# Kernel tuning notes

Hardware: AMD Instinct MI355X
Metric: run time of the kernel (lower is better)

## Reference

```python
import jax, jax.numpy as jnp
import numpy as np

DIM = 128
N_ROUNDS = 120


def _mlp(x, W1, b1, W2, b2, W3, b3):
    h = jax.nn.relu(x @ W1.T + b1)
    h = jax.nn.relu(h @ W2.T + b2)
    return h @ W3.T + b3


def _lstm(x, h, c, Wih, Whh, bih, bhh):
    # torch nn.LSTM gate order: i, f, g, o
    g = x @ Wih.T + h @ Whh.T + (bih + bhh)
    i, f, gg, o = jnp.split(g, 4, axis=-1)
    c2 = jax.nn.sigmoid(f) * c + jax.nn.sigmoid(i) * jnp.tanh(gg)
    h2 = jax.nn.sigmoid(o) * jnp.tanh(c2)
    return h2, c2


def setup_inputs() -> dict:
    key = jax.random.key(0)
    keys = iter(jax.random.split(key, 64))
    def w(*shape):
        return jax.random.normal(next(keys), shape, dtype=jnp.float32) * 0.05
    n_nodes, n_vars = 8000, 1000
    N = n_nodes + n_vars
    # sparse 0/1 adjacency, stored dense as in the original (adj_matrix.values)
    adj = (jax.random.uniform(next(keys), (n_nodes, N)) < 0.003).astype(jnp.float32)
    values = jax.random.randint(next(keys), (N,), 0, 2)
    inp = dict(adj=adj, values=values, n_nodes=n_nodes)
    inp.update(true_W=w(DIM, 1), true_b=w(DIM), false_W=w(DIM, 1), false_b=w(DIM))
    for p in ("cm", "pm"):
        inp.update({p + "_W1": w(DIM, DIM), p + "_b1": w(DIM),
                    p + "_W2": w(DIM, DIM), p + "_b2": w(DIM),
                    p + "_W3": w(DIM, DIM), p + "_b3": w(DIM)})
    inp.update(vv_W1=w(DIM, DIM), vv_b1=w(DIM), vv_W2=w(DIM, DIM), vv_b2=w(DIM),
               vv_W3=w(1, DIM), vv_b3=w(1))
    for p in ("vu", "nu"):
        inp.update({p + "_Wih": w(4 * DIM, DIM), p + "_Whh": w(4 * DIM, DIM),
                    p + "_bih": w(4 * DIM), p + "_bhh": w(4 * DIM)})
    return inp


def reference(adj, values, n_nodes, true_W, true_b, false_W, false_b,
              cm_W1, cm_b1, cm_W2, cm_b2, cm_W3, cm_b3,
              pm_W1, pm_b1, pm_W2, pm_b2, pm_W3, pm_b3,
              vv_W1, vv_b1, vv_W2, vv_b2, vv_W3, vv_b3,
              vu_Wih, vu_Whh, vu_bih, vu_bhh,
              nu_Wih, nu_Whh, nu_bih, nu_bhh):
    init_ts = jnp.ones((1,), jnp.float32)
    true_vec = true_W @ init_ts + true_b     # (128,)
    false_vec = false_W @ init_ts + false_b  # (128,)
    h0 = jnp.where((values == 1)[:, None], true_vec, false_vec)  # (N,128)
    c0 = jnp.zeros_like(h0)

    def step(carry, _):
        h, c = carry
        var_pre = _mlp(h, cm_W1, cm_b1, cm_W2, cm_b2, cm_W3, cm_b3)   # (N,128)
        c2p = adj @ var_pre                                           # (n_nodes,128)
        hn, cn = _lstm(c2p, h[:n_nodes], c[:n_nodes], vu_Wih, vu_Whh, vu_bih, vu_bhh)
        h = jnp.concatenate([hn, h[n_nodes:]], axis=0)
        c = jnp.concatenate([cn, c[n_nodes:]], axis=0)
        node_pre = _mlp(h[:n_nodes], pm_W1, pm_b1, pm_W2, pm_b2, pm_W3, pm_b3)
        p2c = adj.T @ node_pre                                        # (N,128)
        h, c = _lstm(p2c, h, c, nu_Wih, nu_Whh, nu_bih, nu_bhh)
        return (h, c), None

    (h, c), _ = jax.lax.scan(step, (h0, c0), None, length=N_ROUNDS)
    vote = _mlp(h[n_nodes:], vv_W1, vv_b1, vv_W2, vv_b2, vv_W3, vv_b3)  # (n_vars,1)
    return vote.squeeze(-1)
```

## Files before the change

### kernel.cpp

```cpp
#include <hip/hip_runtime.h>
#include <cstddef>
#include <cstdint>

#define DIM 128
#define NROUNDS 120
#define NNZ_CAP (1 << 20)

typedef _Float16 half8 __attribute__((ext_vector_type(8)));
typedef float f32x4 __attribute__((ext_vector_type(4)));
typedef unsigned long long u64;

__device__ __forceinline__ float sigf(float x) { return 1.f / (1.f + __expf(-x)); }
__device__ __forceinline__ float tanh_fast(float x) { return 2.f / (1.f + __expf(-2.f * x)) - 1.f; }

__global__ void count_nz_kernel(const float* __restrict__ adj, int* __restrict__ row_cnt,
                                int* __restrict__ col_cnt, int ncols) {
  int i = blockIdx.x;
  int j = blockIdx.y * blockDim.x + threadIdx.x;
  bool nz = (j < ncols) && (adj[(size_t)i * ncols + j] != 0.f);
  unsigned long long m = __ballot(nz);
  if ((threadIdx.x & 63) == 0) {
    int c = __popcll(m);
    if (c) atomicAdd(&row_cnt[i], c);
  }
  if (nz) atomicAdd(&col_cnt[j], 1);
}

__global__ void scan_kernel(const int* __restrict__ cnt, int* __restrict__ ptr, int n) {
  __shared__ int sdata[256];
  int t = threadIdx.x;
  int per = (n + 255) / 256;
  int beg = t * per;
  int end = beg + per; if (end > n) end = n;
  int local = 0;
  for (int i = beg; i < end; ++i) local += cnt[i];
  sdata[t] = local;
  __syncthreads();
  for (int off = 1; off < 256; off <<= 1) {
    int v = (t >= off) ? sdata[t - off] : 0;
    __syncthreads();
    sdata[t] += v;
    __syncthreads();
  }
  int run = sdata[t] - local;
  for (int i = beg; i < end; ++i) { ptr[i] = run; run += cnt[i]; }
  if (t == 255) ptr[n] = sdata[255];
}

__global__ __launch_bounds__(64) void fill_csr_kernel(const float* __restrict__ adj,
                                                      const int* __restrict__ row_ptr,
                                                      int* __restrict__ col_idx, int ncols) {
  int row = blockIdx.x;
  int lane = threadIdx.x;
  int base = row_ptr[row];
  int cursor = 0;
  const float* arow = adj + (size_t)row * ncols;
  for (int j0 = 0; j0 < ncols; j0 += 64) {
    int j = j0 + lane;
    bool nz = (j < ncols) && (arow[j] != 0.f);
    u64 m = __ballot(nz);
    int pre = __popcll(m & ((1ull << lane) - 1));
    if (nz) col_idx[base + cursor + pre] = j;
    cursor += __popcll(m);
  }
}

__global__ __launch_bounds__(64) void fill_csc_kernel(const float* __restrict__ adj,
                                                      const int* __restrict__ col_ptr,
                                                      int* __restrict__ row_idx,
                                                      int nrows, int ncols) {
  int c = blockIdx.x * 64 + threadIdx.x;
  if (c >= ncols) return;
  int cur = col_ptr[c];
  for (int i = 0; i < nrows; ++i) {
    if (adj[(size_t)i * ncols + c] != 0.f) row_idx[cur++] = i;
  }
}

__global__ void pack_w_kernel(const float* __restrict__ src, int out_dim,
                              _Float16* __restrict__ dh) {
  int idx = blockIdx.x * 256 + threadIdx.x;
  if (idx >= out_dim * DIM) return;
  int n = idx >> 7, k = idx & 127;
  _Float16 hi = (_Float16)src[idx];
  int nt = n >> 4, ks = k >> 5;
  int L = ((k >> 3) & 3) * 16 + (n & 15);
  int j = k & 7;
  dh[((nt * 4 + ks) * 64 + L) * 8 + j] = hi;
}

__global__ void pack_bias_kernel(const float* __restrict__ a, const float* __restrict__ b,
                                 float* __restrict__ o, int n) {
  int i = blockIdx.x * 256 + threadIdx.x;
  if (i < n) o[i] = a[i] + b[i];
}

__global__ void init_hc_kernel(const int* __restrict__ values, const float* __restrict__ tW,
                               const float* __restrict__ tb, const float* __restrict__ fW,
                               const float* __restrict__ fb, float* __restrict__ h,
                               float* __restrict__ c, int N) {
  int idx = blockIdx.x * blockDim.x + threadIdx.x;
  if (idx >= N * DIM) return;
  int row = idx >> 7, col = idx & (DIM - 1);
  float tv = tW[col] + tb[col];
  float fv = fW[col] + fb[col];
  h[idx] = (values[row] == 1) ? tv : fv;
  c[idx] = 0.f;
}

__device__ __forceinline__ int sw_idx(int m, int k) {
  return (m << 7) + (((((k >> 3) ^ (m & 15))) << 3) | (k & 7));
}

__device__ __forceinline__ float touch(const _Float16* __restrict__ w, int n, int tid) {
  float t = 0.f;
  for (int i = tid * 64; i < n; i += 512 * 64) t += (float)w[i];
  return t;
}

template <int NSUB>
__device__ __forceinline__ void stage_rows_t(const float* __restrict__ src, int rend, int rb,
                                             _Float16* Sh, _Float16* Sl, int tid) {
  int seg = tid & 15;
  for (int r = tid >> 4; r < NSUB * 16; r += 32) {
    int row = rb + r;
    float4 v0, v1;
    if (row < rend) {
      const float4* s = (const float4*)(src + (size_t)row * DIM + seg * 8);
      v0 = s[0]; v1 = s[1];
    } else {
      v0.x = v0.y = v0.z = v0.w = 0.f; v1 = v0;
    }
    int a = sw_idx(r, seg * 8);
    float vv[8] = {v0.x, v0.y, v0.z, v0.w, v1.x, v1.y, v1.z, v1.w};
#pragma unroll
    for (int e = 0; e < 8; ++e) {
      _Float16 hi = (_Float16)vv[e];
      Sh[a + e] = hi;
      Sl[a + e] = (_Float16)(vv[e] - (float)hi);
    }
  }
}

template <int NSUB>
__device__ __forceinline__ void gather_rows_t(const int* __restrict__ ptr,
                                              const int* __restrict__ nzidx,
                                              const _Float16* __restrict__ va, int rend, int rb,
                                              _Float16* Xh, _Float16* Xl, int tid) {
  int seg = tid & 15;
  for (int r = tid >> 4; r < NSUB * 16; r += 32) {
    int row = rb + r;
    float a[8];
#pragma unroll
    for (int e = 0; e < 8; ++e) a[e] = 0.f;
    if (row < rend) {
      int s = ptr[row], e_ = ptr[row + 1];
      int p = s;
      for (; p + 8 <= e_; p += 8) {
        half8 v0 = *(const half8*)(va + (size_t)nzidx[p] * DIM + seg * 8);
        half8 v1 = *(const half8*)(va + (size_t)nzidx[p + 1] * DIM + seg * 8);
        half8 v2 = *(const half8*)(va + (size_t)nzidx[p + 2] * DIM + seg * 8);
        half8 v3 = *(const half8*)(va + (size_t)nzidx[p + 3] * DIM + seg * 8);
        half8 v4 = *(const half8*)(va + (size_t)nzidx[p + 4] * DIM + seg * 8);
        half8 v5 = *(const half8*)(va + (size_t)nzidx[p + 5] * DIM + seg * 8);
        half8 v6 = *(const half8*)(va + (size_t)nzidx[p + 6] * DIM + seg * 8);
        half8 v7 = *(const half8*)(va + (size_t)nzidx[p + 7] * DIM + seg * 8);
#pragma unroll
        for (int e = 0; e < 8; ++e)
          a[e] += (((float)v0[e] + (float)v1[e]) + ((float)v2[e] + (float)v3[e])) +
                  (((float)v4[e] + (float)v5[e]) + ((float)v6[e] + (float)v7[e]));
      }
      for (; p + 2 <= e_; p += 2) {
        half8 v0 = *(const half8*)(va + (size_t)nzidx[p] * DIM + seg * 8);
        half8 v1 = *(const half8*)(va + (size_t)nzidx[p + 1] * DIM + seg * 8);
#pragma unroll
        for (int e = 0; e < 8; ++e) a[e] += (float)v0[e] + (float)v1[e];
      }
      if (p < e_) {
        half8 v = *(const half8*)(va + (size_t)nzidx[p] * DIM + seg * 8);
#pragma unroll
        for (int e = 0; e < 8; ++e) a[e] += (float)v[e];
      }
    }
    int aoff = sw_idx(r, seg * 8);
#pragma unroll
    for (int e = 0; e < 8; ++e) {
      _Float16 hi = (_Float16)a[e];
      Xh[aoff + e] = hi;
      Xl[aoff + e] = (_Float16)(a[e] - (float)hi);
    }
  }
}

__device__ __forceinline__ void mfma2(f32x4& acc, half8 ah, half8 al, half8 bh) {
  acc = __builtin_amdgcn_mfma_f32_16x16x32_f16(ah, bh, acc, 0, 0, 0);
  acc = __builtin_amdgcn_mfma_f32_16x16x32_f16(al, bh, acc, 0, 0, 0);
}

template <int NSUB>
__device__ __forceinline__ void mlp_layer_t(const _Float16* Ah_, const _Float16* Al_,
                                            const _Float16* __restrict__ Wh,
                                            const float* __restrict__ B,
                                            _Float16* Dh, _Float16* Dl, int tid) {
  int lane = tid & 63, w = tid >> 6;
  int m16 = lane & 15, quad = lane >> 4;
  float bv = B[w * 16 + m16];
  f32x4 acc[NSUB];
#pragma unroll
  for (int s = 0; s < NSUB; ++s) acc[s] = (f32x4){bv, bv, bv, bv};
#pragma unroll
  for (int ks = 0; ks < 4; ++ks) {
    int boff = ((w * 4 + ks) * 64 + lane) * 8;
    half8 bh = *(const half8*)(Wh + boff);
#pragma unroll
    for (int s = 0; s < NSUB; ++s) {
      int a_off = sw_idx(s * 16 + m16, ks * 32 + quad * 8);
      mfma2(acc[s], *(const half8*)(Ah_ + a_off), *(const half8*)(Al_ + a_off), bh);
    }
  }
#pragma unroll
  for (int s = 0; s < NSUB; ++s)
#pragma unroll
    for (int reg = 0; reg < 4; ++reg) {
      int rl = s * 16 + quad * 4 + reg;
      int col = w * 16 + m16;
      float x = fmaxf(acc[s][reg], 0.f);
      _Float16 hi = (_Float16)x;
      int a = sw_idx(rl, col);
      Dh[a] = hi;
      Dl[a] = (_Float16)(x - (float)hi);
    }
  __syncthreads();
}

template <int NSUB>
__device__ __forceinline__ void mlp_from_lds_t(
    _Float16* S0, _Float16* S1, _Float16* S2, _Float16* S3, int rend, int rb,
    const _Float16* __restrict__ W1h, const float* __restrict__ b1,
    const _Float16* __restrict__ W2h, const float* __restrict__ b2,
    const _Float16* __restrict__ W3h, const float* __restrict__ b3,
    _Float16* __restrict__ out) {
  int tid = threadIdx.x;
  mlp_layer_t<NSUB>(S0, S1, W1h, b1, S2, S3, tid);
  mlp_layer_t<NSUB>(S2, S3, W2h, b2, S0, S1, tid);
  int lane = tid & 63, w = tid >> 6;
  int m16 = lane & 15, quad = lane >> 4;
  float bv = b3[w * 16 + m16];
  f32x4 acc[NSUB];
#pragma unroll
  for (int s = 0; s < NSUB; ++s) acc[s] = (f32x4){bv, bv, bv, bv};
#pragma unroll
  for (int ks = 0; ks < 4; ++ks) {
    int boff = ((w * 4 + ks) * 64 + lane) * 8;
    half8 bh = *(const half8*)(W3h + boff);
#pragma unroll
    for (int s = 0; s < NSUB; ++s) {
      int a_off = sw_idx(s * 16 + m16, ks * 32 + quad * 8);
      mfma2(acc[s], *(const half8*)(S0 + a_off), *(const half8*)(S1 + a_off), bh);
    }
  }
#pragma unroll
  for (int s = 0; s < NSUB; ++s)
#pragma unroll
    for (int reg = 0; reg < 4; ++reg) {
      int row = rb + s * 16 + quad * 4 + reg;
      int col = w * 16 + m16;
      if (row < rend) out[(size_t)row * DIM + col] = (_Float16)acc[s][reg];
    }
}

template <int NSUB>
__global__ __launch_bounds__(512, 4) void mlp3_mfma(
    const float* __restrict__ X, int M, int rpb,
    const _Float16* __restrict__ W1h, const float* __restrict__ b1,
    const _Float16* __restrict__ W2h, const float* __restrict__ b2,
    const _Float16* __restrict__ W3h, const float* __restrict__ b3,
    _Float16* __restrict__ out) {
  __shared__ _Float16 S0[NSUB * 2048], S1[NSUB * 2048], S2[NSUB * 2048], S3[NSUB * 2048];
  int tid = threadIdx.x;
  int rb = blockIdx.x * rpb;
  int rend = rb + rpb; if (rend > M) rend = M;
  float tpf = touch(W1h, DIM * DIM, tid) + touch(W2h, DIM * DIM, tid) + touch(W3h, DIM * DIM, tid);
  stage_rows_t<NSUB>(X, rend, rb, S0, S1, tid);
  asm volatile("" :: "v"(tpf));
  __syncthreads();
  mlp_from_lds_t<NSUB>(S0, S1, S2, S3, rend, rb, W1h, b1, W2h, b2, W3h, b3, out);
}

template <int NSUB, bool DO_MLP>
__global__ __launch_bounds__(512, 4) void lstm_fused(
    const int* __restrict__ ptr, const int* __restrict__ nzidx, const _Float16* __restrict__ va_in,
    float* __restrict__ hbuf, float* __restrict__ cbuf, int M, int rpb,
    const _Float16* __restrict__ Wxh, const _Float16* __restrict__ Whh_,
    const float* __restrict__ bcomb,
    const _Float16* __restrict__ W1h, const float* __restrict__ b1,
    const _Float16* __restrict__ W2h, const float* __restrict__ b2,
    const _Float16* __restrict__ W3h, const float* __restrict__ b3,
    _Float16* __restrict__ va_out) {
  __shared__ _Float16 Xh[NSUB * 2048], Xl[NSUB * 2048], Hh[NSUB * 2048], Hl[NSUB * 2048];
  int tid = threadIdx.x;
  int rb = blockIdx.x * rpb;
  int rend = rb + rpb; if (rend > M) rend = M;

  float tpf = touch(Wxh, 4 * DIM * DIM, tid) + touch(Whh_, 4 * DIM * DIM, tid) +
              touch(W1h, DIM * DIM, tid) + touch(W2h, DIM * DIM, tid) + touch(W3h, DIM * DIM, tid);

  stage_rows_t<NSUB>(hbuf, rend, rb, Hh, Hl, tid);
  gather_rows_t<NSUB>(ptr, nzidx, va_in, rend, rb, Xh, Xl, tid);

  int lane = tid & 63, w = tid >> 6;
  int m16 = lane & 15, quad = lane >> 4;

  float cold[NSUB][4];
#pragma unroll
  for (int s = 0; s < NSUB; ++s)
#pragma unroll
    for (int reg = 0; reg < 4; ++reg) {
      int row = rb + s * 16 + quad * 4 + reg;
      cold[s][reg] = (row < rend) ? cbuf[(size_t)row * DIM + w * 16 + m16] : 0.f;
    }
  asm volatile("" :: "v"(tpf));
  __syncthreads();

  f32x4 acc[NSUB][4];
#pragma unroll
  for (int g = 0; g < 4; ++g) {
    float bv = bcomb[g * 128 + w * 16 + m16];
#pragma unroll
    for (int s = 0; s < NSUB; ++s) acc[s][g] = (f32x4){bv, bv, bv, bv};
  }
#pragma unroll
  for (int ks = 0; ks < 4; ++ks) {
#pragma unroll
    for (int g = 0; g < 4; ++g) {
      int ct = g * 8 + w;
      int boff = ((ct * 4 + ks) * 64 + lane) * 8;
      half8 bh = *(const half8*)(Whh_ + boff);
#pragma unroll
      for (int s = 0; s < NSUB; ++s) {
        int a_off = sw_idx(s * 16 + m16, ks * 32 + quad * 8);
        mfma2(acc[s][g], *(const half8*)(Hh + a_off), *(const half8*)(Hl + a_off), bh);
      }
    }
  }
#pragma unroll
  for (int ks = 0; ks < 4; ++ks) {
#pragma unroll
    for (int g = 0; g < 4; ++g) {
      int ct = g * 8 + w;
      int boff = ((ct * 4 + ks) * 64 + lane) * 8;
      half8 bh = *(const half8*)(Wxh + boff);
#pragma unroll
      for (int s = 0; s < NSUB; ++s) {
        int a_off = sw_idx(s * 16 + m16, ks * 32 + quad * 8);
        mfma2(acc[s][g], *(const half8*)(Xh + a_off), *(const half8*)(Xl + a_off), bh);
      }
    }
  }

  if (DO_MLP) __syncthreads();

#pragma unroll
  for (int s = 0; s < NSUB; ++s)
#pragma unroll
    for (int reg = 0; reg < 4; ++reg) {
      int rl = s * 16 + quad * 4 + reg;
      int row = rb + rl;
      int col = w * 16 + m16;
      float hn = 0.f;
      if (row < rend) {
        float iv = sigf(acc[s][0][reg]);
        float fv = sigf(acc[s][1][reg]);
        float gv = tanh_fast(acc[s][2][reg]);
        float ov = sigf(acc[s][3][reg]);
        size_t o = (size_t)row * DIM + col;
        float cn = fv * cold[s][reg] + iv * gv;
        cbuf[o] = cn;
        hn = ov * tanh_fast(cn);
        hbuf[o] = hn;
      }
      if (DO_MLP) {
        int a = sw_idx(rl, col);
        _Float16 hi = (_Float16)hn;
        Xh[a] = hi;
        Xl[a] = (_Float16)(hn - (float)hi);
      }
    }
  if (DO_MLP) {
    __syncthreads();
    mlp_from_lds_t<NSUB>(Xh, Xl, Hh, Hl, rend, rb, W1h, b1, W2h, b2, W3h, b3, va_out);
  }
}

__device__ __forceinline__ void tile_gemm(const float* S, const float* __restrict__ W,
                                          int colB, int rowB, float acc[4][4]) {
#pragma unroll 4
  for (int kc = 0; kc < DIM; kc += 4) {
    float4 xv[4], wv[4];
#pragma unroll
    for (int r = 0; r < 4; ++r) xv[r] = *(const float4*)(S + (rowB + r) * DIM + kc);
#pragma unroll
    for (int c = 0; c < 4; ++c) wv[c] = *(const float4*)(W + (size_t)(colB + c) * DIM + kc);
#pragma unroll
    for (int r = 0; r < 4; ++r)
#pragma unroll
      for (int c = 0; c < 4; ++c)
        acc[r][c] += xv[r].x * wv[c].x + xv[r].y * wv[c].y + xv[r].z * wv[c].z + xv[r].w * wv[c].w;
  }
}

__device__ __forceinline__ void layer_lds(const float* Sin, float* Sout,
                                          const float* __restrict__ W, const float* __restrict__ B,
                                          bool relu, int colB, int rowB) {
  float acc[4][4];
#pragma unroll
  for (int r = 0; r < 4; ++r)
#pragma unroll
    for (int cc = 0; cc < 4; ++cc) acc[r][cc] = B[colB + cc];
  tile_gemm(Sin, W, colB, rowB, acc);
#pragma unroll
  for (int r = 0; r < 4; ++r) {
    float4 v;
    v.x = acc[r][0]; v.y = acc[r][1]; v.z = acc[r][2]; v.w = acc[r][3];
    if (relu) { v.x = fmaxf(v.x, 0.f); v.y = fmaxf(v.y, 0.f); v.z = fmaxf(v.z, 0.f); v.w = fmaxf(v.w, 0.f); }
    *(float4*)&Sout[(rowB + r) * DIM + colB] = v;
  }
  __syncthreads();
}

__global__ __launch_bounds__(256) void vote_kernel(
    const float* __restrict__ X, int M,
    const float* __restrict__ W1, const float* __restrict__ b1,
    const float* __restrict__ W2, const float* __restrict__ b2,
    const float* __restrict__ W3, const float* __restrict__ b3,
    float* __restrict__ out) {
  __shared__ float Xs[32 * DIM];
  __shared__ float Ys[32 * DIM];
  int tid = threadIdx.x;
  int rb = blockIdx.x * 32;
  int mrows = M - rb; if (mrows > 32) mrows = 32;
  {
    const float4* src = (const float4*)(X + (size_t)rb * DIM);
    float4* dst = (float4*)Xs;
    int nf4 = mrows * (DIM / 4);
    for (int t = tid; t < 32 * (DIM / 4); t += 256) {
      float4 v;
      if (t < nf4) v = src[t];
      else { v.x = v.y = v.z = v.w = 0.f; }
      dst[t] = v;
    }
  }
  __syncthreads();
  int tx = tid & 31, ty = tid >> 5;
  int colB = tx * 4, rowB = ty * 4;
  layer_lds(Xs, Ys, W1, b1, true, colB, rowB);
  layer_lds(Ys, Xs, W2, b2, true, colB, rowB);
  if (tid < 32) {
    int gr = rb + tid;
    if (gr < M) {
      float s = b3[0];
      for (int k = 0; k < DIM; ++k) s += Xs[tid * DIM + k] * W3[k];
      out[gr] = s;
    }
  }
}

#define SZ128 (DIM * DIM)
#define SZ512 (4 * DIM * DIM)
#define O_CM1 0
#define O_CM2 (SZ128)
#define O_CM3 (2 * SZ128)
#define O_PM1 (3 * SZ128)
#define O_PM2 (4 * SZ128)
#define O_PM3 (5 * SZ128)
#define O_VUX ((size_t)6 * SZ128)
#define O_VUH ((size_t)6 * SZ128 + SZ512)
#define O_NUX ((size_t)6 * SZ128 + 2 * SZ512)
#define O_NUH ((size_t)6 * SZ128 + 3 * SZ512)

extern "C" void kernel_launch(void* const* d_in, const int* in_sizes, int n_in,
                              void* d_out, int out_size, void* d_ws, size_t ws_size,
                              hipStream_t stream) {
  const float* adj    = (const float*)d_in[0];
  const int*   values = (const int*)d_in[1];
  const int N       = in_sizes[1];
  const int n_nodes = in_sizes[0] / N;
  const int n_vars  = N - n_nodes;

  const float* true_W  = (const float*)d_in[3];
  const float* true_b  = (const float*)d_in[4];
  const float* false_W = (const float*)d_in[5];
  const float* false_b = (const float*)d_in[6];
  const float* cm_W1 = (const float*)d_in[7];
  const float* cm_b1 = (const float*)d_in[8];
  const float* cm_W2 = (const float*)d_in[9];
  const float* cm_b2 = (const float*)d_in[10];
  const float* cm_W3 = (const float*)d_in[11];
  const float* cm_b3 = (const float*)d_in[12];
  const float* pm_W1 = (const float*)d_in[13];
  const float* pm_b1 = (const float*)d_in[14];
  const float* pm_W2 = (const float*)d_in[15];
  const float* pm_b2 = (const float*)d_in[16];
  const float* pm_W3 = (const float*)d_in[17];
  const float* pm_b3 = (const float*)d_in[18];
  const float* vv_W1 = (const float*)d_in[19];
  const float* vv_b1 = (const float*)d_in[20];
  const float* vv_W2 = (const float*)d_in[21];
  const float* vv_b2 = (const float*)d_in[22];
  const float* vv_W3 = (const float*)d_in[23];
  const float* vv_b3 = (const float*)d_in[24];
  const float* vu_Wih = (const float*)d_in[25];
  const float* vu_Whh = (const float*)d_in[26];
  const float* vu_bih = (const float*)d_in[27];
  const float* vu_bhh = (const float*)d_in[28];
  const float* nu_Wih = (const float*)d_in[29];
  const float* nu_Whh = (const float*)d_in[30];
  const float* nu_bih = (const float*)d_in[31];
  const float* nu_bhh = (const float*)d_in[32];

  uintptr_t p = (uintptr_t)d_ws;
  auto take = [&](size_t bytes) -> void* {
    uintptr_t cur = (p + 255) & ~(uintptr_t)255;
    p = cur + bytes;
    return (void*)cur;
  };
  float* h   = (float*)take((size_t)N * DIM * sizeof(float));
  float* cb  = (float*)take((size_t)N * DIM * sizeof(float));
  _Float16* va1 = (_Float16*)take((size_t)N * DIM * sizeof(_Float16));
  _Float16* va2 = (_Float16*)take((size_t)N * DIM * sizeof(_Float16));
  int* row_ptr = (int*)take((size_t)(n_nodes + 1) * sizeof(int));
  int* col_ptr = (int*)take((size_t)(N + 1) * sizeof(int));
  int* cnts    = (int*)take((size_t)(n_nodes + N) * sizeof(int));
  int* row_cnt = cnts;
  int* col_cnt = cnts + n_nodes;
  int* col_idx = (int*)take((size_t)NNZ_CAP * sizeof(int));
  int* row_idx = (int*)take((size_t)NNZ_CAP * sizeof(int));

  size_t tot_pack = (size_t)6 * SZ128 + (size_t)4 * SZ512;
  _Float16* packh = (_Float16*)take(tot_pack * sizeof(_Float16));
  float* vu_b = (float*)take(512 * sizeof(float));
  float* nu_b = (float*)take(512 * sizeof(float));

  hipMemsetAsync(cnts, 0, (size_t)(n_nodes + N) * sizeof(int), stream);
  dim3 cgrid(n_nodes, (N + 255) / 256);
  count_nz_kernel<<<cgrid, 256, 0, stream>>>(adj, row_cnt, col_cnt, N);
  scan_kernel<<<1, 256, 0, stream>>>(row_cnt, row_ptr, n_nodes);
  scan_kernel<<<1, 256, 0, stream>>>(col_cnt, col_ptr, N);
  fill_csr_kernel<<<n_nodes, 64, 0, stream>>>(adj, row_ptr, col_idx, N);
  fill_csc_kernel<<<(N + 63) / 64, 64, 0, stream>>>(adj, col_ptr, row_idx, n_nodes, N);
  init_hc_kernel<<<(N * DIM + 255) / 256, 256, 0, stream>>>(values, true_W, true_b,
                                                            false_W, false_b, h, cb, N);

  auto pack = [&](const float* src, int out_dim, size_t o) {
    pack_w_kernel<<<(out_dim * DIM + 255) / 256, 256, 0, stream>>>(src, out_dim, packh + o);
  };
  pack(cm_W1, DIM, O_CM1); pack(cm_W2, DIM, O_CM2); pack(cm_W3, DIM, O_CM3);
  pack(pm_W1, DIM, O_PM1); pack(pm_W2, DIM, O_PM2); pack(pm_W3, DIM, O_PM3);
  pack(vu_Wih, 4 * DIM, O_VUX); pack(vu_Whh, 4 * DIM, O_VUH);
  pack(nu_Wih, 4 * DIM, O_NUX); pack(nu_Whh, 4 * DIM, O_NUH);
  pack_bias_kernel<<<2, 256, 0, stream>>>(vu_bih, vu_bhh, vu_b, 512);
  pack_bias_kernel<<<2, 256, 0, stream>>>(nu_bih, nu_bhh, nu_b, 512);

  int rpbN = (N + 499) / 500;
  int gridN = (N + rpbN - 1) / rpbN;
  int rpbn = (n_nodes + 499) / 500;
  int gridn = (n_nodes + rpbn - 1) / rpbn;

  mlp3_mfma<2><<<gridN, 512, 0, stream>>>(h, N, rpbN,
      packh + O_CM1, cm_b1, packh + O_CM2, cm_b2, packh + O_CM3, cm_b3, va1);

  for (int r = 0; r < NROUNDS; ++r) {
    lstm_fused<1, true><<<gridn, 512, 0, stream>>>(row_ptr, col_idx, va1, h, cb, n_nodes, rpbn,
        packh + O_VUX, packh + O_VUH, vu_b,
        packh + O_PM1, pm_b1, packh + O_PM2, pm_b2, packh + O_PM3, pm_b3, va2);
    if (r + 1 < NROUNDS) {
      lstm_fused<2, true><<<gridN, 512, 0, stream>>>(col_ptr, row_idx, va2, h, cb, N, rpbN,
          packh + O_NUX, packh + O_NUH, nu_b,
          packh + O_CM1, cm_b1, packh + O_CM2, cm_b2, packh + O_CM3, cm_b3, va1);
    } else {
      lstm_fused<2, false><<<gridN, 512, 0, stream>>>(col_ptr, row_idx, va2, h, cb, N, rpbN,
          packh + O_NUX, packh + O_NUH, nu_b,
          packh + O_CM1, cm_b1, packh + O_CM2, cm_b2, packh + O_CM3, cm_b3, va1);
    }
  }

  vote_kernel<<<(n_vars + 31) / 32, 256, 0, stream>>>(h + (size_t)n_nodes * DIM, n_vars,
      vv_W1, vv_b1, vv_W2, vv_b2, vv_W3, vv_b3, (float*)d_out);
}
```

Measured before the change: 10.05 ms.

## Replace per-round kernel launches with a persistent kernel using grid barriers

```diff
diff --git a/kernel.cpp b/kernel.cpp
--- a/kernel.cpp
+++ b/kernel.cpp
@@ -5,6 +5,7 @@
 #define DIM 128
 #define NROUNDS 120
 #define NNZ_CAP (1 << 20)
+#define NB 250
 
 typedef _Float16 half8 __attribute__((ext_vector_type(8)));
 typedef float f32x4 __attribute__((ext_vector_type(4)));
@@ -16,14 +17,23 @@
 __global__ void count_nz_kernel(const float* __restrict__ adj, int* __restrict__ row_cnt,
                                 int* __restrict__ col_cnt, int ncols) {
   int i = blockIdx.x;
-  int j = blockIdx.y * blockDim.x + threadIdx.x;
-  bool nz = (j < ncols) && (adj[(size_t)i * ncols + j] != 0.f);
-  unsigned long long m = __ballot(nz);
-  if ((threadIdx.x & 63) == 0) {
-    int c = __popcll(m);
-    if (c) atomicAdd(&row_cnt[i], c);
-  }
-  if (nz) atomicAdd(&col_cnt[j], 1);
+  int t4 = blockIdx.y * blockDim.x + threadIdx.x;
+  int j0 = t4 * 4;
+  int c = 0;
+  if (j0 < ncols) {
+    if ((ncols & 3) == 0) {
+      float4 v = *(const float4*)(adj + (size_t)i * ncols + j0);
+      if (v.x != 0.f) { atomicAdd(&col_cnt[j0 + 0], 1); ++c; }
+      if (v.y != 0.f) { atomicAdd(&col_cnt[j0 + 1], 1); ++c; }
+      if (v.z != 0.f) { atomicAdd(&col_cnt[j0 + 2], 1); ++c; }
+      if (v.w != 0.f) { atomicAdd(&col_cnt[j0 + 3], 1); ++c; }
+    } else {
+      for (int e = 0; e < 4 && j0 + e < ncols; ++e)
+        if (adj[(size_t)i * ncols + j0 + e] != 0.f) { atomicAdd(&col_cnt[j0 + e], 1); ++c; }
+    }
+  }
+  for (int off = 32; off; off >>= 1) c += __shfl_down(c, off, 64);
+  if ((threadIdx.x & 63) == 0 && c) atomicAdd(&row_cnt[i], c);
 }
 
 __global__ void scan_kernel(const int* __restrict__ cnt, int* __restrict__ ptr, int n) {
@@ -47,9 +57,16 @@
   if (t == 255) ptr[n] = sdata[255];
 }
 
-__global__ __launch_bounds__(64) void fill_csr_kernel(const float* __restrict__ adj,
-                                                      const int* __restrict__ row_ptr,
-                                                      int* __restrict__ col_idx, int ncols) {
+__global__ void copy_int_kernel(const int* __restrict__ a, int* __restrict__ b, int n) {
+  int i = blockIdx.x * 256 + threadIdx.x;
+  if (i < n) b[i] = a[i];
+}
+
+__global__ __launch_bounds__(64) void fill_csr_csc_kernel(const float* __restrict__ adj,
+                                                          const int* __restrict__ row_ptr,
+                                                          int* __restrict__ col_idx,
+                                                          int* __restrict__ col_cur,
+                                                          int* __restrict__ row_idx, int ncols) {
   int row = blockIdx.x;
   int lane = threadIdx.x;
   int base = row_ptr[row];
@@ -60,20 +77,12 @@
     bool nz = (j < ncols) && (arow[j] != 0.f);
     u64 m = __ballot(nz);
     int pre = __popcll(m & ((1ull << lane) - 1));
-    if (nz) col_idx[base + cursor + pre] = j;
+    if (nz) {
+      col_idx[base + cursor + pre] = j;
+      int t = atomicAdd(&col_cur[j], 1);
+      row_idx[t] = row;
+    }
     cursor += __popcll(m);
-  }
-}
-
-__global__ __launch_bounds__(64) void fill_csc_kernel(const float* __restrict__ adj,
-                                                      const int* __restrict__ col_ptr,
-                                                      int* __restrict__ row_idx,
-                                                      int nrows, int ncols) {
-  int c = blockIdx.x * 64 + threadIdx.x;
-  if (c >= ncols) return;
-  int cur = col_ptr[c];
-  for (int i = 0; i < nrows; ++i) {
-    if (adj[(size_t)i * ncols + c] != 0.f) row_idx[cur++] = i;
   }
 }
 
@@ -95,19 +104,6 @@
   if (i < n) o[i] = a[i] + b[i];
 }
 
-__global__ void init_hc_kernel(const int* __restrict__ values, const float* __restrict__ tW,
-                               const float* __restrict__ tb, const float* __restrict__ fW,
-                               const float* __restrict__ fb, float* __restrict__ h,
-                               float* __restrict__ c, int N) {
-  int idx = blockIdx.x * blockDim.x + threadIdx.x;
-  if (idx >= N * DIM) return;
-  int row = idx >> 7, col = idx & (DIM - 1);
-  float tv = tW[col] + tb[col];
-  float fv = fW[col] + fb[col];
-  h[idx] = (values[row] == 1) ? tv : fv;
-  c[idx] = 0.f;
-}
-
 __device__ __forceinline__ int sw_idx(int m, int k) {
   return (m << 7) + (((((k >> 3) ^ (m & 15))) << 3) | (k & 7));
 }
@@ -118,42 +114,18 @@
   return t;
 }
 
-template <int NSUB>
-__device__ __forceinline__ void stage_rows_t(const float* __restrict__ src, int rend, int rb,
-                                             _Float16* Sh, _Float16* Sl, int tid) {
+template <int NS>
+__device__ __forceinline__ void gather_pers(const int* __restrict__ ptr,
+                                            const int* __restrict__ nzidx,
+                                            const _Float16* __restrict__ va, int rowlim,
+                                            int b, int nb, _Float16* Xh, _Float16* Xl, int tid) {
   int seg = tid & 15;
-  for (int r = tid >> 4; r < NSUB * 16; r += 32) {
-    int row = rb + r;
-    float4 v0, v1;
-    if (row < rend) {
-      const float4* s = (const float4*)(src + (size_t)row * DIM + seg * 8);
-      v0 = s[0]; v1 = s[1];
-    } else {
-      v0.x = v0.y = v0.z = v0.w = 0.f; v1 = v0;
-    }
-    int a = sw_idx(r, seg * 8);
-    float vv[8] = {v0.x, v0.y, v0.z, v0.w, v1.x, v1.y, v1.z, v1.w};
-#pragma unroll
-    for (int e = 0; e < 8; ++e) {
-      _Float16 hi = (_Float16)vv[e];
-      Sh[a + e] = hi;
-      Sl[a + e] = (_Float16)(vv[e] - (float)hi);
-    }
-  }
-}
-
-template <int NSUB>
-__device__ __forceinline__ void gather_rows_t(const int* __restrict__ ptr,
-                                              const int* __restrict__ nzidx,
-                                              const _Float16* __restrict__ va, int rend, int rb,
-                                              _Float16* Xh, _Float16* Xl, int tid) {
-  int seg = tid & 15;
-  for (int r = tid >> 4; r < NSUB * 16; r += 32) {
-    int row = rb + r;
+  for (int r = tid >> 4; r < NS * 16; r += 32) {
+    int row = b + r * nb;
     float a[8];
 #pragma unroll
     for (int e = 0; e < 8; ++e) a[e] = 0.f;
-    if (row < rend) {
+    if (row < rowlim) {
       int s = ptr[row], e_ = ptr[row + 1];
       int p = s;
       for (; p + 8 <= e_; p += 8) {
@@ -197,7 +169,7 @@
   acc = __builtin_amdgcn_mfma_f32_16x16x32_f16(al, bh, acc, 0, 0, 0);
 }
 
-template <int NSUB>
+template <int NS>
 __device__ __forceinline__ void mlp_layer_t(const _Float16* Ah_, const _Float16* Al_,
                                             const _Float16* __restrict__ Wh,
                                             const float* __restrict__ B,
@@ -205,21 +177,21 @@
   int lane = tid & 63, w = tid >> 6;
   int m16 = lane & 15, quad = lane >> 4;
   float bv = B[w * 16 + m16];
-  f32x4 acc[NSUB];
-#pragma unroll
-  for (int s = 0; s < NSUB; ++s) acc[s] = (f32x4){bv, bv, bv, bv};
+  f32x4 acc[NS];
+#pragma unroll
+  for (int s = 0; s < NS; ++s) acc[s] = (f32x4){bv, bv, bv, bv};
 #pragma unroll
   for (int ks = 0; ks < 4; ++ks) {
     int boff = ((w * 4 + ks) * 64 + lane) * 8;
     half8 bh = *(const half8*)(Wh + boff);
 #pragma unroll
-    for (int s = 0; s < NSUB; ++s) {
+    for (int s = 0; s < NS; ++s) {
       int a_off = sw_idx(s * 16 + m16, ks * 32 + quad * 8);
       mfma2(acc[s], *(const half8*)(Ah_ + a_off), *(const half8*)(Al_ + a_off), bh);
     }
   }
 #pragma unroll
-  for (int s = 0; s < NSUB; ++s)
+  for (int s = 0; s < NS; ++s)
 #pragma unroll
     for (int reg = 0; reg < 4; ++reg) {
       int rl = s * 16 + quad * 4 + reg;
@@ -233,162 +205,262 @@
   __syncthreads();
 }
 
-template <int NSUB>
-__device__ __forceinline__ void mlp_from_lds_t(
-    _Float16* S0, _Float16* S1, _Float16* S2, _Float16* S3, int rend, int rb,
-    const _Float16* __restrict__ W1h, const float* __restrict__ b1,
-    const _Float16* __restrict__ W2h, const float* __restrict__ b2,
-    const _Float16* __restrict__ W3h, const float* __restrict__ b3,
-    _Float16* __restrict__ out) {
-  int tid = threadIdx.x;
-  mlp_layer_t<NSUB>(S0, S1, W1h, b1, S2, S3, tid);
-  mlp_layer_t<NSUB>(S2, S3, W2h, b2, S0, S1, tid);
+template <int NS>
+__device__ __forceinline__ void mlp_pers(const _Float16* Ah, const _Float16* Al,
+                                         _Float16* T1h, _Float16* T1l,
+                                         _Float16* T2h, _Float16* T2l,
+                                         const _Float16* __restrict__ W1h, const float* __restrict__ b1,
+                                         const _Float16* __restrict__ W2h, const float* __restrict__ b2,
+                                         const _Float16* __restrict__ W3h, const float* __restrict__ b3,
+                                         _Float16* __restrict__ out, int rowlim, int b, int nb,
+                                         int tid) {
+  mlp_layer_t<NS>(Ah, Al, W1h, b1, T1h, T1l, tid);
+  mlp_layer_t<NS>(T1h, T1l, W2h, b2, T2h, T2l, tid);
   int lane = tid & 63, w = tid >> 6;
   int m16 = lane & 15, quad = lane >> 4;
   float bv = b3[w * 16 + m16];
-  f32x4 acc[NSUB];
-#pragma unroll
-  for (int s = 0; s < NSUB; ++s) acc[s] = (f32x4){bv, bv, bv, bv};
+  f32x4 acc[NS];
+#pragma unroll
+  for (int s = 0; s < NS; ++s) acc[s] = (f32x4){bv, bv, bv, bv};
 #pragma unroll
   for (int ks = 0; ks < 4; ++ks) {
     int boff = ((w * 4 + ks) * 64 + lane) * 8;
     half8 bh = *(const half8*)(W3h + boff);
 #pragma unroll
-    for (int s = 0; s < NSUB; ++s) {
+    for (int s = 0; s < NS; ++s) {
       int a_off = sw_idx(s * 16 + m16, ks * 32 + quad * 8);
-      mfma2(acc[s], *(const half8*)(S0 + a_off), *(const half8*)(S1 + a_off), bh);
-    }
-  }
-#pragma unroll
-  for (int s = 0; s < NSUB; ++s)
+      mfma2(acc[s], *(const half8*)(T2h + a_off), *(const half8*)(T2l + a_off), bh);
+    }
+  }
+#pragma unroll
+  for (int s = 0; s < NS; ++s)
 #pragma unroll
     for (int reg = 0; reg < 4; ++reg) {
-      int row = rb + s * 16 + quad * 4 + reg;
+      int rl = s * 16 + quad * 4 + reg;
+      int row = b + rl * nb;
       int col = w * 16 + m16;
-      if (row < rend) out[(size_t)row * DIM + col] = (_Float16)acc[s][reg];
-    }
-}
-
-template <int NSUB>
-__global__ __launch_bounds__(512, 4) void mlp3_mfma(
-    const float* __restrict__ X, int M, int rpb,
-    const _Float16* __restrict__ W1h, const float* __restrict__ b1,
-    const _Float16* __restrict__ W2h, const float* __restrict__ b2,
-    const _Float16* __restrict__ W3h, const float* __restrict__ b3,
-    _Float16* __restrict__ out) {
-  __shared__ _Float16 S0[NSUB * 2048], S1[NSUB * 2048], S2[NSUB * 2048], S3[NSUB * 2048];
-  int tid = threadIdx.x;
-  int rb = blockIdx.x * rpb;
-  int rend = rb + rpb; if (rend > M) rend = M;
-  float tpf = touch(W1h, DIM * DIM, tid) + touch(W2h, DIM * DIM, tid) + touch(W3h, DIM * DIM, tid);
-  stage_rows_t<NSUB>(X, rend, rb, S0, S1, tid);
-  asm volatile("" :: "v"(tpf));
-  __syncthreads();
-  mlp_from_lds_t<NSUB>(S0, S1, S2, S3, rend, rb, W1h, b1, W2h, b2, W3h, b3, out);
-}
-
-template <int NSUB, bool DO_MLP>
-__global__ __launch_bounds__(512, 4) void lstm_fused(
-    const int* __restrict__ ptr, const int* __restrict__ nzidx, const _Float16* __restrict__ va_in,
-    float* __restrict__ hbuf, float* __restrict__ cbuf, int M, int rpb,
-    const _Float16* __restrict__ Wxh, const _Float16* __restrict__ Whh_,
-    const float* __restrict__ bcomb,
-    const _Float16* __restrict__ W1h, const float* __restrict__ b1,
-    const _Float16* __restrict__ W2h, const float* __restrict__ b2,
-    const _Float16* __restrict__ W3h, const float* __restrict__ b3,
-    _Float16* __restrict__ va_out) {
-  __shared__ _Float16 Xh[NSUB * 2048], Xl[NSUB * 2048], Hh[NSUB * 2048], Hl[NSUB * 2048];
-  int tid = threadIdx.x;
-  int rb = blockIdx.x * rpb;
-  int rend = rb + rpb; if (rend > M) rend = M;
-
-  float tpf = touch(Wxh, 4 * DIM * DIM, tid) + touch(Whh_, 4 * DIM * DIM, tid) +
-              touch(W1h, DIM * DIM, tid) + touch(W2h, DIM * DIM, tid) + touch(W3h, DIM * DIM, tid);
-
-  stage_rows_t<NSUB>(hbuf, rend, rb, Hh, Hl, tid);
-  gather_rows_t<NSUB>(ptr, nzidx, va_in, rend, rb, Xh, Xl, tid);
-
+      if (row < rowlim) out[(size_t)row * DIM + col] = (_Float16)acc[s][reg];
+    }
+}
+
+template <int NS>
+__device__ __forceinline__ void lstm_pers(const _Float16* Hh, const _Float16* Hl,
+                                          const _Float16* Xh, const _Float16* Xl,
+                                          const _Float16* __restrict__ Wxh,
+                                          const _Float16* __restrict__ Whh_,
+                                          const float* __restrict__ bcomb, int tid,
+                                          f32x4 (&acc)[NS][4]) {
   int lane = tid & 63, w = tid >> 6;
   int m16 = lane & 15, quad = lane >> 4;
-
-  float cold[NSUB][4];
-#pragma unroll
-  for (int s = 0; s < NSUB; ++s)
-#pragma unroll
-    for (int reg = 0; reg < 4; ++reg) {
-      int row = rb + s * 16 + quad * 4 + reg;
-      cold[s][reg] = (row < rend) ? cbuf[(size_t)row * DIM + w * 16 + m16] : 0.f;
-    }
-  asm volatile("" :: "v"(tpf));
-  __syncthreads();
-
-  f32x4 acc[NSUB][4];
 #pragma unroll
   for (int g = 0; g < 4; ++g) {
     float bv = bcomb[g * 128 + w * 16 + m16];
 #pragma unroll
-    for (int s = 0; s < NSUB; ++s) acc[s][g] = (f32x4){bv, bv, bv, bv};
+    for (int s = 0; s < NS; ++s) acc[s][g] = (f32x4){bv, bv, bv, bv};
   }
 #pragma unroll
   for (int ks = 0; ks < 4; ++ks) {
+    half8 ah[NS], al[NS];
+#pragma unroll
+    for (int s = 0; s < NS; ++s) {
+      int a_off = sw_idx(s * 16 + m16, ks * 32 + quad * 8);
+      ah[s] = *(const half8*)(Hh + a_off);
+      al[s] = *(const half8*)(Hl + a_off);
+    }
 #pragma unroll
     for (int g = 0; g < 4; ++g) {
-      int ct = g * 8 + w;
-      int boff = ((ct * 4 + ks) * 64 + lane) * 8;
+      int boff = (((g * 8 + w) * 4 + ks) * 64 + lane) * 8;
       half8 bh = *(const half8*)(Whh_ + boff);
 #pragma unroll
-      for (int s = 0; s < NSUB; ++s) {
-        int a_off = sw_idx(s * 16 + m16, ks * 32 + quad * 8);
-        mfma2(acc[s][g], *(const half8*)(Hh + a_off), *(const half8*)(Hl + a_off), bh);
-      }
-    }
-  }
-#pragma unroll
-  for (int ks = 0; ks < 4; ++ks) {
+      for (int s = 0; s < NS; ++s) mfma2(acc[s][g], ah[s], al[s], bh);
+    }
+#pragma unroll
+    for (int s = 0; s < NS; ++s) {
+      int a_off = sw_idx(s * 16 + m16, ks * 32 + quad * 8);
+      ah[s] = *(const half8*)(Xh + a_off);
+      al[s] = *(const half8*)(Xl + a_off);
+    }
 #pragma unroll
     for (int g = 0; g < 4; ++g) {
-      int ct = g * 8 + w;
-      int boff = ((ct * 4 + ks) * 64 + lane) * 8;
+      int boff = (((g * 8 + w) * 4 + ks) * 64 + lane) * 8;
       half8 bh = *(const half8*)(Wxh + boff);
 #pragma unroll
-      for (int s = 0; s < NSUB; ++s) {
-        int a_off = sw_idx(s * 16 + m16, ks * 32 + quad * 8);
-        mfma2(acc[s][g], *(const half8*)(Xh + a_off), *(const half8*)(Xl + a_off), bh);
-      }
-    }
-  }
-
-  if (DO_MLP) __syncthreads();
-
-#pragma unroll
-  for (int s = 0; s < NSUB; ++s)
+      for (int s = 0; s < NS; ++s) mfma2(acc[s][g], ah[s], al[s], bh);
+    }
+  }
+}
+
+__device__ __forceinline__ void gbar(unsigned* __restrict__ cnt, int nblocks, unsigned ep) {
+  __syncthreads();
+  if (threadIdx.x == 0) {
+    __threadfence();
+    __hip_atomic_fetch_add(cnt, 1u, __ATOMIC_RELAXED, __HIP_MEMORY_SCOPE_AGENT);
+    unsigned tgt = ep * (unsigned)nblocks;
+    int guard = 0;
+    while (__hip_atomic_load(cnt, __ATOMIC_RELAXED, __HIP_MEMORY_SCOPE_AGENT) < tgt) {
+      __builtin_amdgcn_s_sleep(8);
+      if (++guard > (1 << 17)) break;
+    }
+    __threadfence();
+  }
+  __syncthreads();
+}
+
+#define SZ128 (DIM * DIM)
+#define SZ512 (4 * DIM * DIM)
+#define O_CM1 0
+#define O_CM2 (SZ128)
+#define O_CM3 (2 * SZ128)
+#define O_PM1 (3 * SZ128)
+#define O_PM2 (4 * SZ128)
+#define O_PM3 (5 * SZ128)
+#define O_VUX ((size_t)6 * SZ128)
+#define O_VUH ((size_t)6 * SZ128 + SZ512)
+#define O_NUX ((size_t)6 * SZ128 + 2 * SZ512)
+#define O_NUH ((size_t)6 * SZ128 + 3 * SZ512)
+
+#define LSLOT (3 * 2048 + 768)
+
+template <int NS1>
+__global__ __launch_bounds__(512, 2) void persist_kernel(
+    const int* __restrict__ row_ptr, const int* __restrict__ col_idx,
+    const int* __restrict__ col_ptr, const int* __restrict__ row_idx,
+    const int* __restrict__ values, const float* __restrict__ tW, const float* __restrict__ tb,
+    const float* __restrict__ fW, const float* __restrict__ fb,
+    const _Float16* __restrict__ packh,
+    const float* __restrict__ vu_b, const float* __restrict__ nu_b,
+    const float* __restrict__ cm_b1, const float* __restrict__ cm_b2,
+    const float* __restrict__ cm_b3, const float* __restrict__ pm_b1,
+    const float* __restrict__ pm_b2, const float* __restrict__ pm_b3,
+    _Float16* __restrict__ va1, _Float16* __restrict__ va2,
+    float* __restrict__ hout, unsigned* __restrict__ bar_cnt,
+    int n_nodes, int N, int nblocks) {
+  __shared__ _Float16 Hh[LSLOT], Hl[LSLOT], Xh[LSLOT], Xl[LSLOT], T2h[LSLOT], T2l[LSLOT];
+  int tid = threadIdx.x, b = blockIdx.x;
+  int lane = tid & 63, w = tid >> 6, m16 = lane & 15, quad = lane >> 4;
+
+  const _Float16* CM1 = packh + O_CM1;
+  const _Float16* CM2 = packh + O_CM2;
+  const _Float16* CM3 = packh + O_CM3;
+  const _Float16* PM1 = packh + O_PM1;
+  const _Float16* PM2 = packh + O_PM2;
+  const _Float16* PM3 = packh + O_PM3;
+  const _Float16* VUX = packh + O_VUX;
+  const _Float16* VUH = packh + O_VUH;
+  const _Float16* NUX = packh + O_NUX;
+  const _Float16* NUH = packh + O_NUH;
+
+  float cold[3][4];
+#pragma unroll
+  for (int s = 0; s < 3; ++s)
 #pragma unroll
     for (int reg = 0; reg < 4; ++reg) {
+      cold[s][reg] = 0.f;
       int rl = s * 16 + quad * 4 + reg;
-      int row = rb + rl;
+      int row = b + rl * nblocks;
       int col = w * 16 + m16;
-      float hn = 0.f;
-      if (row < rend) {
-        float iv = sigf(acc[s][0][reg]);
-        float fv = sigf(acc[s][1][reg]);
-        float gv = tanh_fast(acc[s][2][reg]);
-        float ov = sigf(acc[s][3][reg]);
-        size_t o = (size_t)row * DIM + col;
-        float cn = fv * cold[s][reg] + iv * gv;
-        cbuf[o] = cn;
-        hn = ov * tanh_fast(cn);
-        hbuf[o] = hn;
-      }
-      if (DO_MLP) {
-        int a = sw_idx(rl, col);
-        _Float16 hi = (_Float16)hn;
-        Xh[a] = hi;
-        Xl[a] = (_Float16)(hn - (float)hi);
-      }
-    }
-  if (DO_MLP) {
+      float hv = 0.f;
+      if (row < N) hv = (values[row] == 1) ? (tW[col] + tb[col]) : (fW[col] + fb[col]);
+      int a = sw_idx(rl, col);
+      _Float16 hi = (_Float16)hv;
+      Hh[a] = hi;
+      Hl[a] = (_Float16)(hv - (float)hi);
+    }
+  __syncthreads();
+
+  unsigned ep = 0;
+  {
+    float tpf = touch(CM1, DIM * DIM, tid) + touch(CM2, DIM * DIM, tid) +
+                touch(CM3, DIM * DIM, tid);
+    asm volatile("" :: "v"(tpf));
+  }
+  mlp_pers<3>(Hh, Hl, Xh, Xl, T2h, T2l, CM1, cm_b1, CM2, cm_b2, CM3, cm_b3,
+              va1, N, b, nblocks, tid);
+  gbar(bar_cnt, nblocks, ++ep);
+
+  for (int r = 0; r < NROUNDS; ++r) {
+    {
+      float tpf = touch(VUX, 4 * DIM * DIM, tid) + touch(VUH, 4 * DIM * DIM, tid) +
+                  touch(PM1, DIM * DIM, tid) + touch(PM2, DIM * DIM, tid) +
+                  touch(PM3, DIM * DIM, tid);
+      gather_pers<NS1>(row_ptr, col_idx, va1, n_nodes, b, nblocks, Xh, Xl, tid);
+      asm volatile("" :: "v"(tpf));
+    }
     __syncthreads();
-    mlp_from_lds_t<NSUB>(Xh, Xl, Hh, Hl, rend, rb, W1h, b1, W2h, b2, W3h, b3, va_out);
+    {
+      f32x4 acc[NS1][4];
+      lstm_pers<NS1>(Hh, Hl, Xh, Xl, VUX, VUH, vu_b, tid, acc);
+      __syncthreads();
+#pragma unroll
+      for (int s = 0; s < NS1; ++s)
+#pragma unroll
+        for (int reg = 0; reg < 4; ++reg) {
+          int rl = s * 16 + quad * 4 + reg;
+          int row = b + rl * nblocks;
+          if (row < n_nodes) {
+            float iv = sigf(acc[s][0][reg]);
+            float fv = sigf(acc[s][1][reg]);
+            float gv = tanh_fast(acc[s][2][reg]);
+            float ov = sigf(acc[s][3][reg]);
+            float cn = fv * cold[s][reg] + iv * gv;
+            cold[s][reg] = cn;
+            float hn = ov * tanh_fast(cn);
+            int a = sw_idx(rl, w * 16 + m16);
+            _Float16 hi = (_Float16)hn;
+            Hh[a] = hi;
+            Hl[a] = (_Float16)(hn - (float)hi);
+          }
+        }
+    }
+    __syncthreads();
+    mlp_pers<NS1>(Hh, Hl, Xh, Xl, T2h, T2l, PM1, pm_b1, PM2, pm_b2, PM3, pm_b3,
+                  va2, n_nodes, b, nblocks, tid);
+    gbar(bar_cnt, nblocks, ++ep);
+
+    bool last = (r == NROUNDS - 1);
+    {
+      float tpf = touch(NUX, 4 * DIM * DIM, tid) + touch(NUH, 4 * DIM * DIM, tid) +
+                  touch(CM1, DIM * DIM, tid) + touch(CM2, DIM * DIM, tid) +
+                  touch(CM3, DIM * DIM, tid);
+      gather_pers<3>(col_ptr, row_idx, va2, N, b, nblocks, Xh, Xl, tid);
+      asm volatile("" :: "v"(tpf));
+    }
+    __syncthreads();
+    {
+      f32x4 acc[3][4];
+      lstm_pers<3>(Hh, Hl, Xh, Xl, NUX, NUH, nu_b, tid, acc);
+      __syncthreads();
+#pragma unroll
+      for (int s = 0; s < 3; ++s)
+#pragma unroll
+        for (int reg = 0; reg < 4; ++reg) {
+          int rl = s * 16 + quad * 4 + reg;
+          int row = b + rl * nblocks;
+          if (row < N) {
+            float iv = sigf(acc[s][0][reg]);
+            float fv = sigf(acc[s][1][reg]);
+            float gv = tanh_fast(acc[s][2][reg]);
+            float ov = sigf(acc[s][3][reg]);
+            float cn = fv * cold[s][reg] + iv * gv;
+            cold[s][reg] = cn;
+            float hn = ov * tanh_fast(cn);
+            if (last) {
+              hout[(size_t)row * DIM + (w * 16 + m16)] = hn;
+            } else {
+              int a = sw_idx(rl, w * 16 + m16);
+              _Float16 hi = (_Float16)hn;
+              Hh[a] = hi;
+              Hl[a] = (_Float16)(hn - (float)hi);
+            }
+          }
+        }
+    }
+    if (!last) {
+      __syncthreads();
+      mlp_pers<3>(Hh, Hl, Xh, Xl, T2h, T2l, CM1, cm_b1, CM2, cm_b2, CM3, cm_b3,
+                  va1, N, b, nblocks, tid);
+      gbar(bar_cnt, nblocks, ++ep);
+    }
   }
 }
 
@@ -464,19 +536,6 @@
     }
   }
 }
-
-#define SZ128 (DIM * DIM)
-#define SZ512 (4 * DIM * DIM)
-#define O_CM1 0
-#define O_CM2 (SZ128)
-#define O_CM3 (2 * SZ128)
-#define O_PM1 (3 * SZ128)
-#define O_PM2 (4 * SZ128)
-#define O_PM3 (5 * SZ128)
-#define O_VUX ((size_t)6 * SZ128)
-#define O_VUH ((size_t)6 * SZ128 + SZ512)
-#define O_NUX ((size_t)6 * SZ128 + 2 * SZ512)
-#define O_NUH ((size_t)6 * SZ128 + 3 * SZ512)
 
 extern "C" void kernel_launch(void* const* d_in, const int* in_sizes, int n_in,
                               void* d_out, int out_size, void* d_ws, size_t ws_size,
@@ -525,7 +584,6 @@
     return (void*)cur;
   };
   float* h   = (float*)take((size_t)N * DIM * sizeof(float));
-  float* cb  = (float*)take((size_t)N * DIM * sizeof(float));
   _Float16* va1 = (_Float16*)take((size_t)N * DIM * sizeof(_Float16));
   _Float16* va2 = (_Float16*)take((size_t)N * DIM * sizeof(_Float16));
   int* row_ptr = (int*)take((size_t)(n_nodes + 1) * sizeof(int));
@@ -533,6 +591,7 @@
   int* cnts    = (int*)take((size_t)(n_nodes + N) * sizeof(int));
   int* row_cnt = cnts;
   int* col_cnt = cnts + n_nodes;
+  int* col_cur = (int*)take((size_t)N * sizeof(int));
   int* col_idx = (int*)take((size_t)NNZ_CAP * sizeof(int));
   int* row_idx = (int*)take((size_t)NNZ_CAP * sizeof(int));
 
@@ -540,16 +599,18 @@
   _Float16* packh = (_Float16*)take(tot_pack * sizeof(_Float16));
   float* vu_b = (float*)take(512 * sizeof(float));
   float* nu_b = (float*)take(512 * sizeof(float));
+  unsigned* bar_cnt = (unsigned*)take(256);
 
   hipMemsetAsync(cnts, 0, (size_t)(n_nodes + N) * sizeof(int), stream);
-  dim3 cgrid(n_nodes, (N + 255) / 256);
+  hipMemsetAsync(bar_cnt, 0, 256, stream);
+
+  int cols4 = (N + 3) / 4;
+  dim3 cgrid(n_nodes, (cols4 + 255) / 256);
   count_nz_kernel<<<cgrid, 256, 0, stream>>>(adj, row_cnt, col_cnt, N);
   scan_kernel<<<1, 256, 0, stream>>>(row_cnt, row_ptr, n_nodes);
   scan_kernel<<<1, 256, 0, stream>>>(col_cnt, col_ptr, N);
-  fill_csr_kernel<<<n_nodes, 64, 0, stream>>>(adj, row_ptr, col_idx, N);
-  fill_csc_kernel<<<(N + 63) / 64, 64, 0, stream>>>(adj, col_ptr, row_idx, n_nodes, N);
-  init_hc_kernel<<<(N * DIM + 255) / 256, 256, 0, stream>>>(values, true_W, true_b,
-                                                            false_W, false_b, h, cb, N);
+  copy_int_kernel<<<(N + 255) / 256, 256, 0, stream>>>(col_ptr, col_cur, N);
+  fill_csr_csc_kernel<<<n_nodes, 64, 0, stream>>>(adj, row_ptr, col_idx, col_cur, row_idx, N);
 
   auto pack = [&](const float* src, int out_dim, size_t o) {
     pack_w_kernel<<<(out_dim * DIM + 255) / 256, 256, 0, stream>>>(src, out_dim, packh + o);
@@ -561,27 +622,17 @@
   pack_bias_kernel<<<2, 256, 0, stream>>>(vu_bih, vu_bhh, vu_b, 512);
   pack_bias_kernel<<<2, 256, 0, stream>>>(nu_bih, nu_bhh, nu_b, 512);
 
-  int rpbN = (N + 499) / 500;
-  int gridN = (N + rpbN - 1) / rpbN;
-  int rpbn = (n_nodes + 499) / 500;
-  int gridn = (n_nodes + rpbn - 1) / rpbn;
-
-  mlp3_mfma<2><<<gridN, 512, 0, stream>>>(h, N, rpbN,
-      packh + O_CM1, cm_b1, packh + O_CM2, cm_b2, packh + O_CM3, cm_b3, va1);
-
-  for (int r = 0; r < NROUNDS; ++r) {
-    lstm_fused<1, true><<<gridn, 512, 0, stream>>>(row_ptr, col_idx, va1, h, cb, n_nodes, rpbn,
-        packh + O_VUX, packh + O_VUH, vu_b,
-        packh + O_PM1, pm_b1, packh + O_PM2, pm_b2, packh + O_PM3, pm_b3, va2);
-    if (r + 1 < NROUNDS) {
-      lstm_fused<2, true><<<gridN, 512, 0, stream>>>(col_ptr, row_idx, va2, h, cb, N, rpbN,
-          packh + O_NUX, packh + O_NUH, nu_b,
-          packh + O_CM1, cm_b1, packh + O_CM2, cm_b2, packh + O_CM3, cm_b3, va1);
-    } else {
-      lstm_fused<2, false><<<gridN, 512, 0, stream>>>(col_ptr, row_idx, va2, h, cb, N, rpbN,
-          packh + O_NUX, packh + O_NUH, nu_b,
-          packh + O_CM1, cm_b1, packh + O_CM2, cm_b2, packh + O_CM3, cm_b3, va1);
-    }
+  int ns1 = (n_nodes + NB * 16 - 1) / (NB * 16);
+  if (ns1 <= 2) {
+    persist_kernel<2><<<NB, 512, 0, stream>>>(
+        row_ptr, col_idx, col_ptr, row_idx, values, true_W, true_b, false_W, false_b,
+        packh, vu_b, nu_b, cm_b1, cm_b2, cm_b3, pm_b1, pm_b2, pm_b3,
+        va1, va2, h, bar_cnt, n_nodes, N, NB);
+  } else {
+    persist_kernel<3><<<NB, 512, 0, stream>>>(
+        row_ptr, col_idx, col_ptr, row_idx, values, true_W, true_b, false_W, false_b,
+        packh, vu_b, nu_b, cm_b1, cm_b2, cm_b3, pm_b1, pm_b2, pm_b3,
+        va1, va2, h, bar_cnt, n_nodes, N, NB);
   }
 
   vote_kernel<<<(n_vars + 31) / 32, 256, 0, stream>>>(h + (size_t)n_nodes * DIM, n_vars,
```

New measurement: 13.88 ms. 38.1% more time.
